# Kernel tuning notes

Measured on AMD Instinct MI355X. Metric: run time of the kernel, lower is better.

## Reference

```python
import jax, jax.numpy as jnp
import numpy as np

TOP_K = 2
N_EXPERTS = 8


def setup_inputs() -> dict:
    key = jax.random.key(0)
    k1, k2, k3 = jax.random.split(key, 3)
    B, S, D, O, E = 2, 4096, 1024, 1024, N_EXPERTS
    scale_in = 1.0 / np.sqrt(D)
    return {
        "x": jax.random.normal(k1, (B, S, D), dtype=jnp.float32),
        "gate_w": jax.random.normal(k2, (E, D), dtype=jnp.float32) * scale_in,
        "gate_b": jnp.zeros((E,), dtype=jnp.float32),
        "expert_w": jax.random.normal(k3, (E, O, D), dtype=jnp.float32) * scale_in,
        "expert_b": jnp.zeros((E, O), dtype=jnp.float32),
    }


def reference(x, gate_w, gate_b, expert_w, expert_b):
    B, S, D = x.shape
    E, O, _ = expert_w.shape
    h = x.reshape(-1, D)  # [T, D] flattened tokens

    # Router: logits -> float32 softmax -> top-k -> renormalized weights
    router_logits = h @ gate_w.T + gate_b  # [T, E]
    probs = jax.nn.softmax(router_logits.astype(jnp.float32), axis=-1)
    topk_w, topk_idx = jax.lax.top_k(probs, TOP_K)  # [T, K]
    topk_w = topk_w / jnp.sum(topk_w, axis=-1, keepdims=True)
    topk_w = topk_w.astype(h.dtype)

    # Dense combine weights per (token, expert): zero for unselected experts.
    combine = jnp.sum(
        jax.nn.one_hot(topk_idx, E, dtype=h.dtype) * topk_w[..., None], axis=1
    )  # [T, E]

    # All-expert outputs, then weighted combine (math-equivalent to
    # per-expert gather-GEMM-scatter since combine is 0 off the top-k).
    expert_out = jnp.einsum("td,eod->teo", h, expert_w) + expert_b[None]  # [T, E, O]
    out = jnp.einsum("te,teo->to", combine, expert_out)  # [T, O]

    return out.reshape(B, S, O), router_logits
```

## Files before the change

### kernel.cpp

```cpp
#include <hip/hip_runtime.h>
#include <hip/hip_bf16.h>
#include <stdint.h>

typedef __attribute__((ext_vector_type(8))) short bf16x8;
typedef __attribute__((ext_vector_type(4))) float f32x4;

#define T_TOKENS 8192
#define DIM 1024
#define ODIM 1024
#define NEXP 8

__device__ __forceinline__ unsigned short f2bf(float f) {
  unsigned u = __float_as_uint(f);
  u = (u + 0x7FFFu + ((u >> 16) & 1u)) >> 16;
  return (unsigned short)u;
}
__device__ __forceinline__ float bf2f(unsigned short h) {
  return __uint_as_float(((unsigned)h) << 16);
}

__global__ __launch_bounds__(256) void router_kernel(
    const float* __restrict__ x, const float* __restrict__ gw, const float* __restrict__ gb,
    float* __restrict__ logits_out, unsigned short* __restrict__ x_bf,
    int* __restrict__ tk_e, float* __restrict__ tk_w) {
  int wave = threadIdx.x >> 6, lane = threadIdx.x & 63;
  int t = blockIdx.x * 4 + wave;
  float acc[NEXP];
#pragma unroll
  for (int e = 0; e < NEXP; ++e) acc[e] = 0.f;
  const float4* xr = (const float4*)(x + (size_t)t * DIM);
  ushort4* xw = (ushort4*)(x_bf + (size_t)t * DIM);
#pragma unroll
  for (int it = 0; it < 4; ++it) {
    int d4 = it * 64 + lane;
    float4 xv = xr[d4];
    ushort4 xb;
    xb.x = f2bf(xv.x); xb.y = f2bf(xv.y); xb.z = f2bf(xv.z); xb.w = f2bf(xv.w);
    xw[d4] = xb;
#pragma unroll
    for (int e = 0; e < NEXP; ++e) {
      float4 gv = ((const float4*)(gw + e * DIM))[d4];
      acc[e] += xv.x * gv.x + xv.y * gv.y + xv.z * gv.z + xv.w * gv.w;
    }
  }
#pragma unroll
  for (int off = 32; off; off >>= 1)
#pragma unroll
    for (int e = 0; e < NEXP; ++e) acc[e] += __shfl_xor(acc[e], off);
  if (lane == 0) {
#pragma unroll
    for (int e = 0; e < NEXP; ++e) acc[e] += gb[e];
    float4 lo = make_float4(acc[0], acc[1], acc[2], acc[3]);
    float4 hi = make_float4(acc[4], acc[5], acc[6], acc[7]);
    float4* lp = (float4*)(logits_out + (size_t)t * NEXP);
    lp[0] = lo; lp[1] = hi;
    int e0 = 0; float l0 = acc[0];
#pragma unroll
    for (int e = 1; e < NEXP; ++e) if (acc[e] > l0) { l0 = acc[e]; e0 = e; }
    int e1 = -1; float l1 = -1e30f;
#pragma unroll
    for (int e = 0; e < NEXP; ++e) if (e != e0 && acc[e] > l1) { l1 = acc[e]; e1 = e; }
    float r = expf(l1 - l0);
    float w0 = 1.f / (1.f + r);
    float w1 = r * w0;
    tk_e[t * 2] = e0; tk_e[t * 2 + 1] = e1;
    tk_w[t * 2] = w0; tk_w[t * 2 + 1] = w1;
  }
}

__global__ __launch_bounds__(1024) void sortconv_kernel(
    const float* __restrict__ ew, unsigned short* __restrict__ w_bf,
    const int* __restrict__ tk_e, const float* __restrict__ tk_w,
    int* __restrict__ offsets_g, int* __restrict__ row_token,
    float* __restrict__ row_weight, int* __restrict__ tk_pos,
    int* __restrict__ tiles_g, int* __restrict__ n_tiles_g) {
  if (blockIdx.x > 0) {
    int i = (blockIdx.x - 1) * 1024 + threadIdx.x;
    float4 v = ((const float4*)ew)[i];
    ushort4 o;
    o.x = f2bf(v.x); o.y = f2bf(v.y); o.z = f2bf(v.z); o.w = f2bf(v.w);
    ((ushort4*)w_bf)[i] = o;
    return;
  }
  int tid = threadIdx.x;
  int lane = tid & 63, wv = tid >> 6;
  __shared__ int wavetot[16][NEXP];
  __shared__ int offs_l[NEXP + 1];

  int pe[16];
  float tw[16];
  const int base = tid * 16;
#pragma unroll
  for (int i = 0; i < 4; ++i) {
    int4 v = ((const int4*)(tk_e + base))[i];
    pe[i * 4 + 0] = v.x; pe[i * 4 + 1] = v.y; pe[i * 4 + 2] = v.z; pe[i * 4 + 3] = v.w;
    float4 w = ((const float4*)(tk_w + base))[i];
    tw[i * 4 + 0] = w.x; tw[i * 4 + 1] = w.y; tw[i * 4 + 2] = w.z; tw[i * 4 + 3] = w.w;
  }
  int h[NEXP];
#pragma unroll
  for (int e = 0; e < NEXP; ++e) h[e] = 0;
#pragma unroll
  for (int i = 0; i < 16; ++i)
#pragma unroll
    for (int e = 0; e < NEXP; ++e) h[e] += (pe[i] == e);

  int incl[NEXP];
#pragma unroll
  for (int e = 0; e < NEXP; ++e) incl[e] = h[e];
#pragma unroll
  for (int off = 1; off < 64; off <<= 1) {
#pragma unroll
    for (int e = 0; e < NEXP; ++e) {
      int n = __shfl_up(incl[e], off);
      if (lane >= off) incl[e] += n;
    }
  }
  if (lane == 63)
#pragma unroll
    for (int e = 0; e < NEXP; ++e) wavetot[wv][e] = incl[e];
  __syncthreads();
  if (tid == 0) {
    int tot[NEXP];
#pragma unroll
    for (int e = 0; e < NEXP; ++e) tot[e] = 0;
    for (int w = 0; w < 16; ++w)
#pragma unroll
      for (int e = 0; e < NEXP; ++e) {
        int v = wavetot[w][e];
        wavetot[w][e] = tot[e];
        tot[e] += v;
      }
    int o = 0;
#pragma unroll
    for (int e = 0; e < NEXP; ++e) { offs_l[e] = o; o += tot[e]; }
    offs_l[NEXP] = o;
    for (int e = 0; e <= NEXP; ++e) offsets_g[e] = offs_l[e];
    int nb = 0;
    for (int e = 0; e < NEXP; ++e) {
      int mt = (tot[e] + 127) >> 7;
      for (int m = 0; m < mt; ++m)
        for (int n = 0; n < 4; ++n) tiles_g[nb++] = e | (n << 4) | (m << 8);
    }
    n_tiles_g[0] = nb;
    n_tiles_g[1] = (nb + 7) >> 3;
  }
  __syncthreads();

  int mybase[NEXP];
#pragma unroll
  for (int e = 0; e < NEXP; ++e) mybase[e] = offs_l[e] + wavetot[wv][e] + (incl[e] - h[e]);
  int run[NEXP];
#pragma unroll
  for (int e = 0; e < NEXP; ++e) run[e] = 0;
#pragma unroll
  for (int i = 0; i < 16; ++i) {
    int pos = 0;
#pragma unroll
    for (int e = 0; e < NEXP; ++e)
      if (pe[i] == e) { pos = mybase[e] + run[e]; run[e]++; }
    int pair = base + i;
    row_token[pos] = pair >> 1;
    row_weight[pos] = tw[i];
    tk_pos[pair] = pos;
  }
}

#define GLOAD16(g, l)                                                                   \
  __builtin_amdgcn_global_load_lds((const __attribute__((address_space(1))) unsigned int*)(g), \
                                   (__attribute__((address_space(3))) unsigned int*)(l), 16, 0, 0)
#define BUFSZ 24576

__global__ __launch_bounds__(512, 4) void gemm_kernel(
    const unsigned short* __restrict__ x_bf, const unsigned short* __restrict__ w_bf,
    const int* __restrict__ row_token, const float* __restrict__ row_weight,
    const int* __restrict__ offsets, const int* __restrict__ tiles,
    const int* __restrict__ n_tiles, unsigned short* __restrict__ tmp) {
  int nb = n_tiles[0], cpx = n_tiles[1];
  int wg = blockIdx.x;
  int slot = wg >> 3;
  if (slot >= cpx) return;
  int idx = (wg & 7) * cpx + slot;
  if (idx >= nb) return;
  int s = tiles[idx];
  int e = s & 7;
  int n0 = ((s >> 4) & 3) << 8;
  int m0 = (s >> 8) << 7;
  int seg0 = offsets[e], segN = offsets[e + 1] - seg0;

  int tid = threadIdx.x;
  int lane = tid & 63, wave = tid >> 6;
  int wr = wave >> 2, wc = wave & 3;

  __shared__ __align__(16) char smem[3 * BUFSZ];

  int arow = tid >> 2;
  int swzc = ((tid & 3) ^ ((tid >> 3) & 3)) << 4;
  int gr0 = m0 + arow; if (gr0 > segN - 1) gr0 = segN - 1;
  const char* srcA = (const char*)x_bf + (size_t)row_token[seg0 + gr0] * 2048 + swzc;
  const char* srcB0 = (const char*)w_bf + (((size_t)e << 20) + (size_t)(n0 + arow) * 1024) * 2 + swzc;
  const char* srcB1 = srcB0 + 128 * 2048;
  const int dA = tid * 16;
  const int dB0 = 8192 + tid * 16;
  const int dB1 = 16384 + tid * 16;

  const int rsw = (((lane >> 4) ^ (lane >> 1)) & 3) << 4;
  int aoff[4], boff[4];
#pragma unroll
  for (int m = 0; m < 4; ++m)
    aoff[m] = (wr * 64 + m * 16 + (lane & 15)) * 64 + rsw;
#pragma unroll
  for (int n = 0; n < 4; ++n)
    boff[n] = 8192 + (wc * 64 + n * 16 + (lane & 15)) * 64 + rsw;

  f32x4 acc[4][4];
#pragma unroll
  for (int m = 0; m < 4; ++m)
#pragma unroll
    for (int n = 0; n < 4; ++n) acc[m][n] = (f32x4){0.f, 0.f, 0.f, 0.f};

#define STAGE3(bufo, kb)                           \
  {                                                \
    GLOAD16(srcA + (kb), smem + (bufo) + dA);      \
    GLOAD16(srcB0 + (kb), smem + (bufo) + dB0);    \
    GLOAD16(srcB1 + (kb), smem + (bufo) + dB1);    \
  }

  STAGE3(0, 0);
  STAGE3(BUFSZ, 64);

  int cb = 0;
  for (int kt = 0; kt < 32; ++kt) {
    if (kt < 31) {
      asm volatile("s_waitcnt vmcnt(3)" ::: "memory");
    } else {
      asm volatile("s_waitcnt vmcnt(0)" ::: "memory");
    }
    __builtin_amdgcn_s_barrier();
    const int cur = cb * BUFSZ;
    bf16x8 a_[4], b_[4];
#pragma unroll
    for (int m = 0; m < 4; ++m) a_[m] = *(const bf16x8*)(smem + cur + aoff[m]);
#pragma unroll
    for (int n = 0; n < 4; ++n) b_[n] = *(const bf16x8*)(smem + cur + boff[n]);
    if (kt < 30) {
      int cbn = cb + 2; if (cbn >= 3) cbn -= 3;
      const int kbn = (kt + 2) * 64;
      STAGE3(cbn * BUFSZ, kbn);
    }
    __builtin_amdgcn_s_setprio(1);
#pragma unroll
    for (int m = 0; m < 4; ++m)
#pragma unroll
      for (int n = 0; n < 4; ++n)
        acc[m][n] = __builtin_amdgcn_mfma_f32_16x16x32_bf16(a_[m], b_[n], acc[m][n], 0, 0, 0);
    __builtin_amdgcn_s_setprio(0);
    cb = (cb + 1 == 3) ? 0 : cb + 1;
  }

#pragma unroll
  for (int m = 0; m < 4; ++m) {
#pragma unroll
    for (int r = 0; r < 4; ++r) {
      int g = m0 + wr * 64 + m * 16 + ((lane >> 4) << 2) + r;
      if (g < segN) {
        int p = seg0 + g;
        float w = row_weight[p];
#pragma unroll
        for (int n = 0; n < 4; ++n) {
          int col = n0 + wc * 64 + n * 16 + (lane & 15);
          tmp[(size_t)p * 1024 + col] = f2bf(acc[m][n][r] * w);
        }
      }
    }
  }
#undef STAGE3
}

__global__ __launch_bounds__(256) void combine_kernel(
    const unsigned short* __restrict__ tmp, const float* __restrict__ eb,
    const int* __restrict__ tk_e, const float* __restrict__ tk_w,
    const int* __restrict__ tk_pos, float* __restrict__ out) {
  int t = blockIdx.x;
  int o = threadIdx.x * 4;
  int p0 = tk_pos[t * 2], p1 = tk_pos[t * 2 + 1];
  int e0 = tk_e[t * 2], e1 = tk_e[t * 2 + 1];
  float w0 = tk_w[t * 2], w1 = tk_w[t * 2 + 1];
  ushort4 a = *(const ushort4*)(tmp + (size_t)p0 * 1024 + o);
  ushort4 b = *(const ushort4*)(tmp + (size_t)p1 * 1024 + o);
  float4 b0 = *(const float4*)(eb + e0 * 1024 + o);
  float4 b1 = *(const float4*)(eb + e1 * 1024 + o);
  float4 r;
  r.x = bf2f(a.x) + bf2f(b.x) + w0 * b0.x + w1 * b1.x;
  r.y = bf2f(a.y) + bf2f(b.y) + w0 * b0.y + w1 * b1.y;
  r.z = bf2f(a.z) + bf2f(b.z) + w0 * b0.z + w1 * b1.z;
  r.w = bf2f(a.w) + bf2f(b.w) + w0 * b0.w + w1 * b1.w;
  *(float4*)(out + (size_t)t * 1024 + o) = r;
}

extern "C" void kernel_launch(void* const* d_in, const int* in_sizes, int n_in,
                              void* d_out, int out_size, void* d_ws, size_t ws_size,
                              hipStream_t stream) {
  const float* x  = (const float*)d_in[0];
  const float* gw = (const float*)d_in[1];
  const float* gb = (const float*)d_in[2];
  const float* ew = (const float*)d_in[3];
  const float* eb = (const float*)d_in[4];
  float* out = (float*)d_out;
  float* logits = out + (size_t)T_TOKENS * ODIM;

  char* ws = (char*)d_ws;
  unsigned short* x_bf = (unsigned short*)(ws);
  unsigned short* w_bf = (unsigned short*)(ws + 16777216);
  unsigned short* tmp  = (unsigned short*)(ws + 33554432);
  int*   tk_e      = (int*)(ws + 67108864);
  float* tk_w      = (float*)(ws + 67174400);
  int*   tk_pos    = (int*)(ws + 67239936);
  int*   row_token = (int*)(ws + 67305472);
  float* row_weight= (float*)(ws + 67371008);
  int*   offsets   = (int*)(ws + 67436544);
  int*   n_tiles   = (int*)(ws + 67436608);
  int*   tiles     = (int*)(ws + 67436672);

  router_kernel<<<2048, 256, 0, stream>>>(x, gw, gb, logits, x_bf, tk_e, tk_w);
  sortconv_kernel<<<2049, 1024, 0, stream>>>(ew, w_bf, tk_e, tk_w, offsets, row_token,
                                             row_weight, tk_pos, tiles, n_tiles);
  gemm_kernel<<<544, 512, 0, stream>>>(x_bf, w_bf, row_token, row_weight, offsets, tiles,
                                       n_tiles, tmp);
  combine_kernel<<<8192, 256, 0, stream>>>(tmp, eb, tk_e, tk_w, tk_pos, out);
}
```

Before: 120.6 us.

## Make expert GEMM persistent with per-XCD atomic tile queues

The grouped GEMM kernel becomes a persistent loop. Each block repeatedly claims a tile index from an atomic counter belonging to its XCD chunk, instead of mapping one tile to each block statically. The sort kernel zeroes the eight counters, and the launch shrinks from 544 to 512 blocks. The aim is to balance the variable tile count across blocks and avoid idle blocks that exit early, at the cost of an atomic plus barrier per tile and some blocks doing tiles serially.

```diff
diff --git a/kernel.cpp b/kernel.cpp
--- a/kernel.cpp
+++ b/kernel.cpp
@@ -144,6 +144,8 @@
     }
     n_tiles_g[0] = nb;
     n_tiles_g[1] = (nb + 7) >> 3;
+#pragma unroll
+    for (int q = 0; q < 8; ++q) n_tiles_g[2 + q] = 0;
   }
   __syncthreads();
 
@@ -175,31 +177,22 @@
     const unsigned short* __restrict__ x_bf, const unsigned short* __restrict__ w_bf,
     const int* __restrict__ row_token, const float* __restrict__ row_weight,
     const int* __restrict__ offsets, const int* __restrict__ tiles,
-    const int* __restrict__ n_tiles, unsigned short* __restrict__ tmp) {
-  int nb = n_tiles[0], cpx = n_tiles[1];
-  int wg = blockIdx.x;
-  int slot = wg >> 3;
-  if (slot >= cpx) return;
-  int idx = (wg & 7) * cpx + slot;
-  if (idx >= nb) return;
-  int s = tiles[idx];
-  int e = s & 7;
-  int n0 = ((s >> 4) & 3) << 8;
-  int m0 = (s >> 8) << 7;
-  int seg0 = offsets[e], segN = offsets[e + 1] - seg0;
-
-  int tid = threadIdx.x;
-  int lane = tid & 63, wave = tid >> 6;
-  int wr = wave >> 2, wc = wave & 3;
+    int* __restrict__ n_tiles, unsigned short* __restrict__ tmp) {
+  const int nb = n_tiles[0], cpx = n_tiles[1];
+  const int chunk = blockIdx.x & 7;
+  const int qbase = chunk * cpx;
+  int qend = qbase + cpx; if (qend > nb) qend = nb;
+  int* qcur = &n_tiles[2 + chunk];
+
+  const int tid = threadIdx.x;
+  const int lane = tid & 63, wave = tid >> 6;
+  const int wr = wave >> 2, wc = wave & 3;
 
   __shared__ __align__(16) char smem[3 * BUFSZ];
-
-  int arow = tid >> 2;
-  int swzc = ((tid & 3) ^ ((tid >> 3) & 3)) << 4;
-  int gr0 = m0 + arow; if (gr0 > segN - 1) gr0 = segN - 1;
-  const char* srcA = (const char*)x_bf + (size_t)row_token[seg0 + gr0] * 2048 + swzc;
-  const char* srcB0 = (const char*)w_bf + (((size_t)e << 20) + (size_t)(n0 + arow) * 1024) * 2 + swzc;
-  const char* srcB1 = srcB0 + 128 * 2048;
+  __shared__ int sh_idx;
+
+  const int arow = tid >> 2;
+  const int swzc = ((tid & 3) ^ ((tid >> 3) & 3)) << 4;
   const int dA = tid * 16;
   const int dB0 = 8192 + tid * 16;
   const int dB1 = 16384 + tid * 16;
@@ -213,11 +206,27 @@
   for (int n = 0; n < 4; ++n)
     boff[n] = 8192 + (wc * 64 + n * 16 + (lane & 15)) * 64 + rsw;
 
-  f32x4 acc[4][4];
-#pragma unroll
-  for (int m = 0; m < 4; ++m)
-#pragma unroll
-    for (int n = 0; n < 4; ++n) acc[m][n] = (f32x4){0.f, 0.f, 0.f, 0.f};
+  for (;;) {
+    if (tid == 0) sh_idx = qbase + atomicAdd(qcur, 1);
+    __syncthreads();
+    const int idx = sh_idx;
+    if (idx >= qend) return;
+    const int s = tiles[idx];
+    const int e = s & 7;
+    const int n0 = ((s >> 4) & 3) << 8;
+    const int m0 = (s >> 8) << 7;
+    const int seg0 = offsets[e], segN = offsets[e + 1] - seg0;
+
+    int gr0 = m0 + arow; if (gr0 > segN - 1) gr0 = segN - 1;
+    const char* srcA = (const char*)x_bf + (size_t)row_token[seg0 + gr0] * 2048 + swzc;
+    const char* srcB0 = (const char*)w_bf + (((size_t)e << 20) + (size_t)(n0 + arow) * 1024) * 2 + swzc;
+    const char* srcB1 = srcB0 + 128 * 2048;
+
+    f32x4 acc[4][4];
+#pragma unroll
+    for (int m = 0; m < 4; ++m)
+#pragma unroll
+      for (int n = 0; n < 4; ++n) acc[m][n] = (f32x4){0.f, 0.f, 0.f, 0.f};
 
 #define STAGE3(bufo, kb)                           \
   {                                                \
@@ -226,55 +235,56 @@
     GLOAD16(srcB1 + (kb), smem + (bufo) + dB1);    \
   }
 
-  STAGE3(0, 0);
-  STAGE3(BUFSZ, 64);
-
-  int cb = 0;
-  for (int kt = 0; kt < 32; ++kt) {
-    if (kt < 31) {
-      asm volatile("s_waitcnt vmcnt(3)" ::: "memory");
-    } else {
-      asm volatile("s_waitcnt vmcnt(0)" ::: "memory");
-    }
-    __builtin_amdgcn_s_barrier();
-    const int cur = cb * BUFSZ;
-    bf16x8 a_[4], b_[4];
-#pragma unroll
-    for (int m = 0; m < 4; ++m) a_[m] = *(const bf16x8*)(smem + cur + aoff[m]);
-#pragma unroll
-    for (int n = 0; n < 4; ++n) b_[n] = *(const bf16x8*)(smem + cur + boff[n]);
-    if (kt < 30) {
-      int cbn = cb + 2; if (cbn >= 3) cbn -= 3;
-      const int kbn = (kt + 2) * 64;
-      STAGE3(cbn * BUFSZ, kbn);
-    }
-    __builtin_amdgcn_s_setprio(1);
-#pragma unroll
-    for (int m = 0; m < 4; ++m)
-#pragma unroll
-      for (int n = 0; n < 4; ++n)
-        acc[m][n] = __builtin_amdgcn_mfma_f32_16x16x32_bf16(a_[m], b_[n], acc[m][n], 0, 0, 0);
-    __builtin_amdgcn_s_setprio(0);
-    cb = (cb + 1 == 3) ? 0 : cb + 1;
-  }
-
-#pragma unroll
-  for (int m = 0; m < 4; ++m) {
-#pragma unroll
-    for (int r = 0; r < 4; ++r) {
-      int g = m0 + wr * 64 + m * 16 + ((lane >> 4) << 2) + r;
-      if (g < segN) {
-        int p = seg0 + g;
-        float w = row_weight[p];
-#pragma unroll
-        for (int n = 0; n < 4; ++n) {
-          int col = n0 + wc * 64 + n * 16 + (lane & 15);
-          tmp[(size_t)p * 1024 + col] = f2bf(acc[m][n][r] * w);
+    STAGE3(0, 0);
+    STAGE3(BUFSZ, 64);
+
+    int cb = 0;
+    for (int kt = 0; kt < 32; ++kt) {
+      if (kt < 31) {
+        asm volatile("s_waitcnt vmcnt(3)" ::: "memory");
+      } else {
+        asm volatile("s_waitcnt vmcnt(0)" ::: "memory");
+      }
+      __builtin_amdgcn_s_barrier();
+      const int cur = cb * BUFSZ;
+      bf16x8 a_[4], b_[4];
+#pragma unroll
+      for (int m = 0; m < 4; ++m) a_[m] = *(const bf16x8*)(smem + cur + aoff[m]);
+#pragma unroll
+      for (int n = 0; n < 4; ++n) b_[n] = *(const bf16x8*)(smem + cur + boff[n]);
+      if (kt < 30) {
+        int cbn = cb + 2; if (cbn >= 3) cbn -= 3;
+        const int kbn = (kt + 2) * 64;
+        STAGE3(cbn * BUFSZ, kbn);
+      }
+      __builtin_amdgcn_s_setprio(1);
+#pragma unroll
+      for (int m = 0; m < 4; ++m)
+#pragma unroll
+        for (int n = 0; n < 4; ++n)
+          acc[m][n] = __builtin_amdgcn_mfma_f32_16x16x32_bf16(a_[m], b_[n], acc[m][n], 0, 0, 0);
+      __builtin_amdgcn_s_setprio(0);
+      cb = (cb + 1 == 3) ? 0 : cb + 1;
+    }
+
+#pragma unroll
+    for (int m = 0; m < 4; ++m) {
+#pragma unroll
+      for (int r = 0; r < 4; ++r) {
+        int g = m0 + wr * 64 + m * 16 + ((lane >> 4) << 2) + r;
+        if (g < segN) {
+          int p = seg0 + g;
+          float w = row_weight[p];
+#pragma unroll
+          for (int n = 0; n < 4; ++n) {
+            int col = n0 + wc * 64 + n * 16 + (lane & 15);
+            tmp[(size_t)p * 1024 + col] = f2bf(acc[m][n][r] * w);
+          }
         }
       }
     }
-  }
 #undef STAGE3
+  }
 }
 
 __global__ __launch_bounds__(256) void combine_kernel(
@@ -325,7 +335,7 @@
   router_kernel<<<2048, 256, 0, stream>>>(x, gw, gb, logits, x_bf, tk_e, tk_w);
   sortconv_kernel<<<2049, 1024, 0, stream>>>(ew, w_bf, tk_e, tk_w, offsets, row_token,
                                              row_weight, tk_pos, tiles, n_tiles);
-  gemm_kernel<<<544, 512, 0, stream>>>(x_bf, w_bf, row_token, row_weight, offsets, tiles,
+  gemm_kernel<<<512, 512, 0, stream>>>(x_bf, w_bf, row_token, row_weight, offsets, tiles,
                                        n_tiles, tmp);
   combine_kernel<<<8192, 256, 0, stream>>>(tmp, eb, tk_e, tk_w, tk_pos, out);
 }
```

Result: slower. 130.6 us (+8.3%).
